# Kernel optimization log

Hardware: AMD Instinct MI355X
Metric: run time of the kernel (lower is better)

The kernel has to match this reference:

```python
import jax, jax.numpy as jnp
import numpy as np

D_MODEL = 1024
N_HEADS = 16
HEAD_DIM = D_MODEL // N_HEADS
ROPE_BASE = 10000.0


def setup_inputs() -> dict:
    key = jax.random.key(0)
    ks = jax.random.split(key, 5)
    B, S = 1, 4096
    scale = 1.0 / np.sqrt(D_MODEL)
    x = jax.random.normal(ks[0], (B, S, D_MODEL), dtype=jnp.float32)
    Wq = jax.random.normal(ks[1], (D_MODEL, D_MODEL), dtype=jnp.float32) * scale
    Wk = jax.random.normal(ks[2], (D_MODEL, D_MODEL), dtype=jnp.float32) * scale
    Wv = jax.random.normal(ks[3], (D_MODEL, D_MODEL), dtype=jnp.float32) * scale
    Wo = jax.random.normal(ks[4], (D_MODEL, D_MODEL), dtype=jnp.float32) * scale
    return {"x": x, "Wq": Wq, "Wk": Wk, "Wv": Wv, "Wo": Wo}


def _rope(q, k):
    # q, k: [B, S, H, Dh]
    S, Dh = q.shape[1], q.shape[-1]
    inv_freq = 1.0 / (ROPE_BASE ** (jnp.arange(0, Dh, 2, dtype=jnp.float32) / Dh))
    t = jnp.arange(S, dtype=jnp.float32)
    freqs = jnp.outer(t, inv_freq)                      # [S, Dh/2]
    emb = jnp.concatenate([freqs, freqs], axis=-1)      # [S, Dh]
    cos = jnp.cos(emb)[None, :, None, :]                # [1, S, 1, Dh]
    sin = jnp.sin(emb)[None, :, None, :]

    def rotate_half(v):
        v1, v2 = v[..., : Dh // 2], v[..., Dh // 2 :]
        return jnp.concatenate([-v2, v1], axis=-1)

    return q * cos + rotate_half(q) * sin, k * cos + rotate_half(k) * sin


def reference(x, Wq, Wk, Wv, Wo):
    B, S, _ = x.shape
    H, Dh = N_HEADS, HEAD_DIM
    # torch Linear: y = x @ W.T
    q = (x @ Wq.T).reshape(B, S, H, Dh)
    k = (x @ Wk.T).reshape(B, S, H, Dh)
    v = (x @ Wv.T).reshape(B, S, H, Dh)
    q, k = _rope(q, k)
    scale = 1.0 / np.sqrt(Dh)
    # scores: [B, H, S, S]
    scores = jnp.einsum("bqhd,bkhd->bhqk", q, k) * scale
    causal = jnp.triu(jnp.ones((S, S), dtype=bool), k=1)
    scores = jnp.where(causal, -jnp.inf, scores)
    attn = jax.nn.softmax(scores, axis=-1)
    out = jnp.einsum("bhqk,bkhd->bqhd", attn, v).reshape(B, S, H * Dh)
    return out @ Wo.T
```

## Files before the change

### kernel.cpp

```cpp
#include <hip/hip_runtime.h>
#include <hip/hip_bf16.h>

typedef __attribute__((ext_vector_type(8))) short bf16x8;
typedef __attribute__((ext_vector_type(4))) float f32x4;
typedef unsigned short u16;

#define S_LEN 4096
#define DM 1024
#define NH 16
#define DH 64
#define PSTR 72

__device__ __forceinline__ u16 f2b_rne(float f) {
  unsigned u = __builtin_bit_cast(unsigned, f);
  return (u16)((u + 0x7fffu + ((u >> 16) & 1u)) >> 16);
}
__device__ __forceinline__ unsigned pk2(float a, float b) {
  unsigned ua = __builtin_bit_cast(unsigned, a);
  unsigned ub = __builtin_bit_cast(unsigned, b);
  ua = (ua + 0x7fffu + ((ua >> 16) & 1u)) >> 16;
  ub = (ub + 0x7fffu + ((ub >> 16) & 1u)) & 0xffff0000u;
  return ua | ub;
}
__device__ __forceinline__ unsigned pk2t(float a, float b) {
  return __builtin_amdgcn_perm(__builtin_bit_cast(unsigned, b),
                               __builtin_bit_cast(unsigned, a), 0x07060302u);
}

__device__ __forceinline__ void glds16(const u16* g, u16* l) {
  __builtin_amdgcn_global_load_lds(
      (const __attribute__((address_space(1))) unsigned int*)g,
      (__attribute__((address_space(3))) unsigned int*)l, 16, 0, 0);
}

__global__ __launch_bounds__(256) void cvt_all(const float* __restrict__ x,
                                               const float* __restrict__ Wq,
                                               const float* __restrict__ Wk,
                                               const float* __restrict__ Wv,
                                               const float* __restrict__ Wo,
                                               u16* __restrict__ xb, u16* __restrict__ wqb,
                                               u16* __restrict__ wkb, u16* __restrict__ wvb,
                                               u16* __restrict__ wob) {
  int idx = (blockIdx.x * 256 + threadIdx.x) * 4;
  const float* src;
  u16* dst;
  int o;
  if (idx < 4194304) {
    src = x; dst = xb; o = idx;
  } else {
    int t = idx - 4194304;
    int wsel = t >> 20;
    o = t & 1048575;
    src = (wsel == 0) ? Wq : (wsel == 1) ? Wk : (wsel == 2) ? Wv : Wo;
    dst = (wsel == 0) ? wqb : (wsel == 1) ? wkb : (wsel == 2) ? wvb : wob;
  }
  float4 v = *(const float4*)(src + o);
  uint2 ov;
  ov.x = pk2(v.x, v.y);
  ov.y = pk2(v.z, v.w);
  *(uint2*)(dst + o) = ov;
}

__global__ __launch_bounds__(256) void zero_kernel(float4* __restrict__ p) {
  p[blockIdx.x * 256 + threadIdx.x] = float4{0.f, 0.f, 0.f, 0.f};
}

__global__ __launch_bounds__(256) void qkv_gemm(const u16* __restrict__ A,
                                                const u16* __restrict__ Wq,
                                                const u16* __restrict__ Wk,
                                                const u16* __restrict__ Wv,
                                                u16* __restrict__ Qo, u16* __restrict__ Ko,
                                                u16* __restrict__ Vt) {
  __shared__ __align__(16) u16 As[2 * 128 * 32];
  __shared__ __align__(16) u16 Bs[2 * 128 * 32];
  const int mat = blockIdx.x >> 3;
  const u16* B = (mat == 0) ? Wq : (mat == 1) ? Wk : Wv;
  const int K = DM, N = DM;
  const int tid = threadIdx.x;
  const int wave = tid >> 6, lane = tid & 63;
  const int fm = lane & 15, fq = lane >> 4;
  const int mb = blockIdx.y * 128, nb = (blockIdx.x & 7) * 128;
  const int wm = (wave & 1) * 64, wn = (wave >> 1) * 64;

  f32x4 acc[4][4];
#pragma unroll
  for (int i = 0; i < 4; ++i)
#pragma unroll
    for (int j = 0; j < 4; ++j)
#pragma unroll
      for (int r = 0; r < 4; ++r) acc[i][j][r] = 0.f;

  const int r_ = tid >> 2;
  const int cg = (tid & 3) ^ ((r_ >> 1) & 3);
  const u16* Ag0 = A + (size_t)(mb + r_) * K + cg * 8;
  const u16* Ag1 = A + (size_t)(mb + r_ + 64) * K + cg * 8;
  const u16* Bg0 = B + (size_t)(nb + r_) * K + cg * 8;
  const u16* Bg1 = B + (size_t)(nb + r_ + 64) * K + cg * 8;
  const int l0 = wave * 512;
  const int l1 = 2048 + wave * 512;
  const int sw = (fm >> 1) & 3;

  int buf = 0;
  glds16(Ag0, As + l0);
  glds16(Ag1, As + l1);
  glds16(Bg0, Bs + l0);
  glds16(Bg1, Bs + l1);

  for (int k0 = 0; k0 < K; k0 += 32) {
    __syncthreads();
    if (k0 + 32 < K) {
      int bo = (buf ^ 1) * 4096;
      glds16(Ag0 + k0 + 32, As + bo + l0);
      glds16(Ag1 + k0 + 32, As + bo + l1);
      glds16(Bg0 + k0 + 32, Bs + bo + l0);
      glds16(Bg1 + k0 + 32, Bs + bo + l1);
    }
    const u16* Ab = As + buf * 4096;
    const u16* Bb = Bs + buf * 4096;
    bf16x8 av[4], bv[4];
#pragma unroll
    for (int t = 0; t < 4; ++t) {
      av[t] = *(const bf16x8*)(Ab + (wm + t * 16 + fm) * 32 + ((fq ^ sw) * 8));
      bv[t] = *(const bf16x8*)(Bb + (wn + t * 16 + fm) * 32 + ((fq ^ sw) * 8));
    }
#pragma unroll
    for (int i = 0; i < 4; ++i)
#pragma unroll
      for (int j = 0; j < 4; ++j)
        acc[i][j] = __builtin_amdgcn_mfma_f32_16x16x32_bf16(av[i], bv[j], acc[i][j], 0, 0, 0);
    buf ^= 1;
  }

  if (mat < 2) {
    u16* Out = (mat == 0) ? Qo : Ko;
    const float qs = (mat == 0) ? 0.1803368801111204f : 1.0f;
    const float c1 = -9.2103403719761836f / 32.f;
    const float if0 = __expf((float)fm * c1);
    const float if1 = __expf((float)(16 + fm) * c1);
#pragma unroll
    for (int ii = 0; ii < 4; ++ii) {
#pragma unroll
      for (int r = 0; r < 4; ++r) {
        float s = (float)(mb + wm + ii * 16 + fq * 4 + r);
#pragma unroll
        for (int jp = 0; jp < 2; ++jp) {
          float ang = s * (jp ? if1 : if0);
          float sn, cs;
          __sincosf(ang, &sn, &cs);
          float a = acc[ii][jp][r], b = acc[ii][jp + 2][r];
          acc[ii][jp][r] = (a * cs - b * sn) * qs;
          acc[ii][jp + 2][r] = (b * cs + a * sn) * qs;
        }
      }
    }
#pragma unroll
    for (int i = 0; i < 4; ++i)
#pragma unroll
      for (int j = 0; j < 4; ++j)
#pragma unroll
        for (int r = 0; r < 4; ++r) {
          int row = mb + wm + i * 16 + fq * 4 + r;
          int col = nb + wn + j * 16 + fm;
          Out[(size_t)row * N + col] = f2b_rne(acc[i][j][r]);
        }
  } else {
#pragma unroll
    for (int i = 0; i < 4; ++i)
#pragma unroll
      for (int j = 0; j < 4; ++j) {
        int col = nb + wn + j * 16 + fm;
        int row0 = mb + wm + i * 16 + fq * 4;
        uint2 pv;
        pv.x = pk2(acc[i][j][0], acc[i][j][1]);
        pv.y = pk2(acc[i][j][2], acc[i][j][3]);
        *(uint2*)(Vt + (size_t)col * S_LEN + row0) = pv;
      }
  }
}

__global__ __launch_bounds__(256) void o_gemm(const u16* __restrict__ A,
                                              const u16* __restrict__ B,
                                              float* __restrict__ C, int M, int N, int K) {
  __shared__ __align__(16) u16 As[2 * 64 * 32];
  __shared__ __align__(16) u16 Bs[2 * 128 * 32];
  const int tid = threadIdx.x;
  const int wave = tid >> 6, lane = tid & 63;
  const int fm = lane & 15, fq = lane >> 4;
  const int mb = blockIdx.y * 64, nb = blockIdx.x * 128;
  const int wm = (wave & 1) * 32, wn = (wave >> 1) * 64;

  f32x4 acc[2][4];
#pragma unroll
  for (int i = 0; i < 2; ++i)
#pragma unroll
    for (int j = 0; j < 4; ++j)
#pragma unroll
      for (int r = 0; r < 4; ++r) acc[i][j][r] = 0.f;

  const int r_ = tid >> 2;
  const int cg = (tid & 3) ^ ((r_ >> 1) & 3);
  const u16* Ag0 = A + (size_t)(mb + r_) * K + cg * 8;
  const u16* Bg0 = B + (size_t)(nb + r_) * K + cg * 8;
  const u16* Bg1 = B + (size_t)(nb + r_ + 64) * K + cg * 8;
  const int l0 = wave * 512;
  const int l1 = 2048 + wave * 512;
  const int sw = (fm >> 1) & 3;

  int buf = 0;
  glds16(Ag0, As + l0);
  glds16(Bg0, Bs + l0);
  glds16(Bg1, Bs + l1);

  for (int k0 = 0; k0 < K; k0 += 32) {
    __syncthreads();
    if (k0 + 32 < K) {
      int aoff = (buf ^ 1) * 2048, boff = (buf ^ 1) * 4096;
      glds16(Ag0 + k0 + 32, As + aoff + l0);
      glds16(Bg0 + k0 + 32, Bs + boff + l0);
      glds16(Bg1 + k0 + 32, Bs + boff + l1);
    }
    const u16* Ab = As + buf * 2048;
    const u16* Bb = Bs + buf * 4096;
    bf16x8 av[2], bv[4];
#pragma unroll
    for (int t = 0; t < 2; ++t)
      av[t] = *(const bf16x8*)(Ab + (wm + t * 16 + fm) * 32 + ((fq ^ sw) * 8));
#pragma unroll
    for (int t = 0; t < 4; ++t)
      bv[t] = *(const bf16x8*)(Bb + (wn + t * 16 + fm) * 32 + ((fq ^ sw) * 8));
#pragma unroll
    for (int i = 0; i < 2; ++i)
#pragma unroll
      for (int j = 0; j < 4; ++j)
        acc[i][j] = __builtin_amdgcn_mfma_f32_16x16x32_bf16(av[i], bv[j], acc[i][j], 0, 0, 0);
    buf ^= 1;
  }
#pragma unroll
  for (int i = 0; i < 2; ++i)
#pragma unroll
    for (int j = 0; j < 4; ++j)
#pragma unroll
      for (int r = 0; r < 4; ++r) {
        int row = mb + wm + i * 16 + fq * 4 + r;
        int col = nb + wn + j * 16 + fm;
        C[(size_t)row * N + col] = acc[i][j][r];
      }
}

template <int STORE>
__global__ __launch_bounds__(512, 4) void attn_kernel(const u16* __restrict__ Q,
                                                      const u16* __restrict__ K,
                                                      const u16* __restrict__ Vt,
                                                      float* __restrict__ Oacc,
                                                      float* __restrict__ Lacc) {
  __shared__ __align__(16) u16 Ks[2 * 4096];
  __shared__ __align__(16) u16 Vs[2 * 4096];
  __shared__ __align__(16) u16 Ps[8][16 * PSTR];
  const int tid = threadIdx.x;
  const int w = tid >> 6, lane = tid & 63;
  const int fm = lane & 15, fq = lane >> 4;
  const int bid = blockIdx.x;
  const int u = bid & 255, hi = bid >> 8;
  const int h = u & 15;
  const int qt0 = u >> 4;
  const int qt = hi ? qt0 : 15 - qt0;
  const int half = hi;
  const int qb = qt * 256 + w * 32;
  const int nlocal = 2 * qt + 2;
  const int kbase = half * nlocal;
  const int dtile = qb >> 6;

  bf16x8 q0[2], q1[2];
#pragma unroll
  for (int g = 0; g < 2; ++g) {
    const u16* qp = Q + (size_t)(qb + g * 16 + fm) * DM + h * DH + fq * 8;
    q0[g] = *(const bf16x8*)(qp);
    q1[g] = *(const bf16x8*)(qp + 32);
  }
  f32x4 o[2][4];
  f32x4 ls[2];
#pragma unroll
  for (int g = 0; g < 2; ++g) {
#pragma unroll
    for (int r = 0; r < 4; ++r) ls[g][r] = 0.f;
#pragma unroll
    for (int c4 = 0; c4 < 4; ++c4)
#pragma unroll
      for (int r = 0; r < 4; ++r) o[g][c4][r] = 0.f;
  }
  const short ONEB = (short)0x3F80;
  const bf16x8 vone = {ONEB, ONEB, ONEB, ONEB, ONEB, ONEB, ONEB, ONEB};

  const int rr = tid >> 3;
  const int cc8 = (tid & 7) ^ (rr & 7);
  const u16* Kg = K + (size_t)rr * DM + h * DH + cc8 * 8;
  const u16* Vg = Vt + (size_t)(h * DH + rr) * S_LEN + cc8 * 8;
  const int l0 = w * 512;
  const int sw7 = fm & 7;
  const f32x4 zf = {0.f, 0.f, 0.f, 0.f};

  glds16(Kg + (size_t)kbase * 64 * DM, Ks + l0);
  glds16(Vg + kbase * 64, Vs + l0);

  int buf = 0;
  for (int kl = 0; kl < nlocal; ++kl) {
    const int ktg = kbase + kl;
    __syncthreads();
    if (kl + 1 < nlocal) {
      int bo = (buf ^ 1) * 4096;
      glds16(Kg + (size_t)(ktg + 1) * 64 * DM, Ks + bo + l0);
      glds16(Vg + (ktg + 1) * 64, Vs + bo + l0);
    }
    if (ktg <= dtile) {
      const u16* Kb = Ks + buf * 4096;
      const u16* Vb = Vs + buf * 4096;

      f32x4 st[2][4];
#pragma unroll
      for (int t = 0; t < 4; ++t) {
        const u16* kr = Kb + (t * 16 + fm) * 64;
        bf16x8 ka = *(const bf16x8*)(kr + ((fq ^ sw7) * 8));
        bf16x8 kb2 = *(const bf16x8*)(kr + (((fq + 4) ^ sw7) * 8));
#pragma unroll
        for (int g = 0; g < 2; ++g) {
          f32x4 s = __builtin_amdgcn_mfma_f32_16x16x32_bf16(ka, q0[g], zf, 0, 0, 0);
          st[g][t] = __builtin_amdgcn_mfma_f32_16x16x32_bf16(kb2, q1[g], s, 0, 0, 0);
        }
      }
      if (ktg == dtile) {
#pragma unroll
        for (int g = 0; g < 2; ++g) {
          int qg = qb + g * 16 + fm;
#pragma unroll
          for (int t = 0; t < 4; ++t) {
            int key = ktg * 64 + t * 16 + fq * 4;
#pragma unroll
            for (int r = 0; r < 4; ++r)
              st[g][t][r] = (key + r > qg) ? -1e30f : st[g][t][r];
          }
        }
      }
      bf16x8 pvb[4][2];
#pragma unroll
      for (int c4 = 0; c4 < 4; ++c4) {
        const u16* vr = Vb + (c4 * 16 + fm) * 64;
        pvb[c4][0] = *(const bf16x8*)(vr + ((fq ^ sw7) * 8));
        pvb[c4][1] = *(const bf16x8*)(vr + (((fq + 4) ^ sw7) * 8));
      }
#pragma unroll
      for (int g = 0; g < 2; ++g) {
#pragma unroll
        for (int t = 0; t < 4; ++t) {
          float p0 = __builtin_amdgcn_exp2f(st[g][t][0]);
          float p1 = __builtin_amdgcn_exp2f(st[g][t][1]);
          float p2 = __builtin_amdgcn_exp2f(st[g][t][2]);
          float p3 = __builtin_amdgcn_exp2f(st[g][t][3]);
          uint2 pk;
          pk.x = pk2t(p0, p1);
          pk.y = pk2t(p2, p3);
          *(uint2*)(&Ps[w][fm * PSTR + t * 16 + fq * 4]) = pk;
        }
        asm volatile("s_waitcnt lgkmcnt(0)" ::: "memory");
        bf16x8 ap0 = *(const bf16x8*)(&Ps[w][fm * PSTR + fq * 8]);
        bf16x8 ap1 = *(const bf16x8*)(&Ps[w][fm * PSTR + 32 + fq * 8]);
        ls[g] = __builtin_amdgcn_mfma_f32_16x16x32_bf16(ap0, vone, ls[g], 0, 0, 0);
        ls[g] = __builtin_amdgcn_mfma_f32_16x16x32_bf16(ap1, vone, ls[g], 0, 0, 0);
#pragma unroll
        for (int c4 = 0; c4 < 4; ++c4) {
          o[g][c4] = __builtin_amdgcn_mfma_f32_16x16x32_bf16(ap0, pvb[c4][0], o[g][c4], 0, 0, 0);
          o[g][c4] = __builtin_amdgcn_mfma_f32_16x16x32_bf16(ap1, pvb[c4][1], o[g][c4], 0, 0, 0);
        }
      }
    }
    buf ^= 1;
  }
  if (STORE) {
    float* Ob = Oacc + (((size_t)half * NH + h) * S_LEN + qt * 256 + w * 32) * DH;
    float* Lb = Lacc + ((size_t)half * NH + h) * S_LEN + qt * 256 + w * 32;
#pragma unroll
    for (int g = 0; g < 2; ++g) {
      if (fm == 0) {
#pragma unroll
        for (int r = 0; r < 4; ++r) Lb[g * 16 + fq * 4 + r] = ls[g][r];
      }
#pragma unroll
      for (int c4 = 0; c4 < 4; ++c4)
#pragma unroll
        for (int r = 0; r < 4; ++r)
          Ob[(size_t)(g * 16 + fq * 4 + r) * DH + c4 * 16 + fm] = o[g][c4][r];
    }
  } else {
    float* Ob = Oacc + ((size_t)h * S_LEN + qt * 256 + w * 32) * DH;
    float* Lb = Lacc + h * S_LEN + qt * 256 + w * 32;
#pragma unroll
    for (int g = 0; g < 2; ++g) {
      if (fm == 0) {
#pragma unroll
        for (int r = 0; r < 4; ++r)
          unsafeAtomicAdd(Lb + g * 16 + fq * 4 + r, ls[g][r]);
      }
#pragma unroll
      for (int c4 = 0; c4 < 4; ++c4)
#pragma unroll
        for (int r = 0; r < 4; ++r)
          unsafeAtomicAdd(Ob + (g * 16 + fq * 4 + r) * DH + c4 * 16 + fm, o[g][c4][r]);
    }
  }
}

__global__ __launch_bounds__(256) void combine2_kernel(const float* __restrict__ O0,
                                                       const float* __restrict__ O1,
                                                       const float* __restrict__ L0,
                                                       const float* __restrict__ L1,
                                                       u16* __restrict__ Ctx) {
  int idx = blockIdx.x * 256 + threadIdx.x;
  int d4 = (idx & 15) * 4;
  int hh = (idx >> 4) & 15;
  int row = idx >> 8;
  size_t ob = ((size_t)hh * S_LEN + row) * DH + d4;
  float4 a = *(const float4*)(O0 + ob);
  float4 b = *(const float4*)(O1 + ob);
  float il = 1.0f / (L0[hh * S_LEN + row] + L1[hh * S_LEN + row]);
  uint2 o;
  o.x = pk2((a.x + b.x) * il, (a.y + b.y) * il);
  o.y = pk2((a.z + b.z) * il, (a.w + b.w) * il);
  *(uint2*)(Ctx + (size_t)row * DM + hh * DH + d4) = o;
}

__global__ __launch_bounds__(256) void combine_kernel(const float* __restrict__ Oacc,
                                                      const float* __restrict__ Lacc,
                                                      u16* __restrict__ Ctx) {
  int idx = blockIdx.x * 256 + threadIdx.x;
  int d4 = (idx & 15) * 4;
  int hh = (idx >> 4) & 15;
  int row = idx >> 8;
  float4 a = *(const float4*)(Oacc + ((size_t)hh * S_LEN + row) * DH + d4);
  float il = 1.0f / Lacc[hh * S_LEN + row];
  uint2 o;
  o.x = pk2(a.x * il, a.y * il);
  o.y = pk2(a.z * il, a.w * il);
  *(uint2*)(Ctx + (size_t)row * DM + hh * DH + d4) = o;
}

extern "C" void kernel_launch(void* const* d_in, const int* in_sizes, int n_in,
                              void* d_out, int out_size, void* d_ws, size_t ws_size,
                              hipStream_t stream) {
  const float* x  = (const float*)d_in[0];
  const float* Wq = (const float*)d_in[1];
  const float* Wk = (const float*)d_in[2];
  const float* Wv = (const float*)d_in[3];
  const float* Wo = (const float*)d_in[4];
  float* out = (float*)d_out;

  const size_t MB = 1u << 20;
  char* ws = (char*)d_ws;

  if (ws_size >= 72 * MB) {
    u16* xb    = (u16*)(ws + 0 * MB);
    u16* wqb   = (u16*)(ws + 8 * MB);
    u16* wkb   = (u16*)(ws + 10 * MB);
    u16* wvb   = (u16*)(ws + 12 * MB);
    u16* wob   = (u16*)(ws + 14 * MB);
    u16* Qb    = (u16*)(ws + 16 * MB);
    u16* Kb    = (u16*)(ws + 24 * MB);
    u16* Vtb   = (u16*)(ws + 32 * MB);
    float* Op  = (float*)(ws + 40 * MB);
    float* Lp  = (float*)(ws + 8 * MB);
    u16* Ctx   = (u16*)(ws + 0 * MB);

    cvt_all<<<8192, 256, 0, stream>>>(x, Wq, Wk, Wv, Wo, xb, wqb, wkb, wvb, wob);
    qkv_gemm<<<dim3(24, 32), 256, 0, stream>>>(xb, wqb, wkb, wvb, Qb, Kb, Vtb);
    attn_kernel<1><<<512, 512, 0, stream>>>(Qb, Kb, Vtb, Op, Lp);
    combine2_kernel<<<4096, 256, 0, stream>>>(Op, Op + (size_t)NH * S_LEN * DH,
                                              Lp, Lp + (size_t)NH * S_LEN, Ctx);
    o_gemm<<<dim3(8, 64), 256, 0, stream>>>(Ctx, wob, out, S_LEN, DM, DM);
  } else {
    u16* xb    = (u16*)(ws + 0 * MB);
    u16* wqb   = (u16*)(ws + 8 * MB);
    u16* wkb   = (u16*)(ws + 10 * MB);
    u16* wvb   = (u16*)(ws + 12 * MB);
    float* Oacc = (float*)(ws + 0 * MB);
    float* Lacc = (float*)(ws + 16 * MB);
    u16* wob   = (u16*)(ws + 17 * MB);
    u16* Qb    = (u16*)(ws + 19 * MB);
    u16* Kb    = (u16*)(ws + 27 * MB);
    u16* Vtb   = (u16*)(ws + 35 * MB);
    u16* Ctx   = (u16*)(ws + 43 * MB);

    cvt_all<<<8192, 256, 0, stream>>>(x, Wq, Wk, Wv, Wo, xb, wqb, wkb, wvb, wob);
    qkv_gemm<<<dim3(24, 32), 256, 0, stream>>>(xb, wqb, wkb, wvb, Qb, Kb, Vtb);
    zero_kernel<<<4160, 256, 0, stream>>>((float4*)Oacc);
    attn_kernel<0><<<512, 512, 0, stream>>>(Qb, Kb, Vtb, Oacc, Lacc);
    combine_kernel<<<4096, 256, 0, stream>>>(Oacc, Lacc, Ctx);
    o_gemm<<<dim3(8, 64), 256, 0, stream>>>(Ctx, wob, out, S_LEN, DM, DM);
  }
}
```

Before: 219.9 us.

## Load K/V fragments directly from global memory instead of LDS double buffer

The attention kernel drops the shared-memory double-buffered K/V staging and its per-iteration block barrier, and instead has each wave load its MFMA operand fragments straight from global memory. Each wave also iterates only up to its own last causal tile, so waves no longer wait on the block for tiles they skip. The trade-off is that the K/V loads, once shared by all eight waves through LDS, are now repeated per wave and served by cache. The loads also have no software prefetch, so global latency is exposed, and the launch-bounds occupancy hint is removed.

```diff
diff --git a/kernel.cpp b/kernel.cpp
--- a/kernel.cpp
+++ b/kernel.cpp
@@ -248,13 +248,11 @@
 }
 
 template <int STORE>
-__global__ __launch_bounds__(512, 4) void attn_kernel(const u16* __restrict__ Q,
-                                                      const u16* __restrict__ K,
-                                                      const u16* __restrict__ Vt,
-                                                      float* __restrict__ Oacc,
-                                                      float* __restrict__ Lacc) {
-  __shared__ __align__(16) u16 Ks[2 * 4096];
-  __shared__ __align__(16) u16 Vs[2 * 4096];
+__global__ __launch_bounds__(512) void attn_kernel(const u16* __restrict__ Q,
+                                                   const u16* __restrict__ K,
+                                                   const u16* __restrict__ Vt,
+                                                   float* __restrict__ Oacc,
+                                                   float* __restrict__ Lacc) {
   __shared__ __align__(16) u16 Ps[8][16 * PSTR];
   const int tid = threadIdx.x;
   const int w = tid >> 6, lane = tid & 63;
@@ -269,6 +267,8 @@
   const int nlocal = 2 * qt + 2;
   const int kbase = half * nlocal;
   const int dtile = qb >> 6;
+  const int kend = kbase + nlocal;
+  const int mylast = (kend - 1 < dtile) ? (kend - 1) : dtile;
 
   bf16x8 q0[2], q1[2];
 #pragma unroll
@@ -290,89 +290,68 @@
   }
   const short ONEB = (short)0x3F80;
   const bf16x8 vone = {ONEB, ONEB, ONEB, ONEB, ONEB, ONEB, ONEB, ONEB};
-
-  const int rr = tid >> 3;
-  const int cc8 = (tid & 7) ^ (rr & 7);
-  const u16* Kg = K + (size_t)rr * DM + h * DH + cc8 * 8;
-  const u16* Vg = Vt + (size_t)(h * DH + rr) * S_LEN + cc8 * 8;
-  const int l0 = w * 512;
-  const int sw7 = fm & 7;
   const f32x4 zf = {0.f, 0.f, 0.f, 0.f};
 
-  glds16(Kg + (size_t)kbase * 64 * DM, Ks + l0);
-  glds16(Vg + kbase * 64, Vs + l0);
-
-  int buf = 0;
-  for (int kl = 0; kl < nlocal; ++kl) {
-    const int ktg = kbase + kl;
-    __syncthreads();
-    if (kl + 1 < nlocal) {
-      int bo = (buf ^ 1) * 4096;
-      glds16(Kg + (size_t)(ktg + 1) * 64 * DM, Ks + bo + l0);
-      glds16(Vg + (ktg + 1) * 64, Vs + bo + l0);
-    }
-    if (ktg <= dtile) {
-      const u16* Kb = Ks + buf * 4096;
-      const u16* Vb = Vs + buf * 4096;
-
-      f32x4 st[2][4];
+  const u16* Kfrag = K + (size_t)fm * DM + h * DH + fq * 8;
+  const u16* Vfrag = Vt + (size_t)(h * DH + fm) * S_LEN + fq * 8;
+
+  for (int ktg = kbase; ktg <= mylast; ++ktg) {
+    f32x4 st[2][4];
+#pragma unroll
+    for (int t = 0; t < 4; ++t) {
+      const u16* kr = Kfrag + (size_t)(ktg * 64 + t * 16) * DM;
+      bf16x8 ka = *(const bf16x8*)(kr);
+      bf16x8 kb2 = *(const bf16x8*)(kr + 32);
+#pragma unroll
+      for (int g = 0; g < 2; ++g) {
+        f32x4 s = __builtin_amdgcn_mfma_f32_16x16x32_bf16(ka, q0[g], zf, 0, 0, 0);
+        st[g][t] = __builtin_amdgcn_mfma_f32_16x16x32_bf16(kb2, q1[g], s, 0, 0, 0);
+      }
+    }
+    if (ktg == dtile) {
+#pragma unroll
+      for (int g = 0; g < 2; ++g) {
+        int qg = qb + g * 16 + fm;
+#pragma unroll
+        for (int t = 0; t < 4; ++t) {
+          int key = ktg * 64 + t * 16 + fq * 4;
+#pragma unroll
+          for (int r = 0; r < 4; ++r)
+            st[g][t][r] = (key + r > qg) ? -1e30f : st[g][t][r];
+        }
+      }
+    }
+    bf16x8 pvb[4][2];
+#pragma unroll
+    for (int c4 = 0; c4 < 4; ++c4) {
+      const u16* vr = Vfrag + (size_t)(c4 * 16) * S_LEN + ktg * 64;
+      pvb[c4][0] = *(const bf16x8*)(vr);
+      pvb[c4][1] = *(const bf16x8*)(vr + 32);
+    }
+#pragma unroll
+    for (int g = 0; g < 2; ++g) {
 #pragma unroll
       for (int t = 0; t < 4; ++t) {
-        const u16* kr = Kb + (t * 16 + fm) * 64;
-        bf16x8 ka = *(const bf16x8*)(kr + ((fq ^ sw7) * 8));
-        bf16x8 kb2 = *(const bf16x8*)(kr + (((fq + 4) ^ sw7) * 8));
-#pragma unroll
-        for (int g = 0; g < 2; ++g) {
-          f32x4 s = __builtin_amdgcn_mfma_f32_16x16x32_bf16(ka, q0[g], zf, 0, 0, 0);
-          st[g][t] = __builtin_amdgcn_mfma_f32_16x16x32_bf16(kb2, q1[g], s, 0, 0, 0);
-        }
-      }
-      if (ktg == dtile) {
-#pragma unroll
-        for (int g = 0; g < 2; ++g) {
-          int qg = qb + g * 16 + fm;
-#pragma unroll
-          for (int t = 0; t < 4; ++t) {
-            int key = ktg * 64 + t * 16 + fq * 4;
-#pragma unroll
-            for (int r = 0; r < 4; ++r)
-              st[g][t][r] = (key + r > qg) ? -1e30f : st[g][t][r];
-          }
-        }
-      }
-      bf16x8 pvb[4][2];
+        float p0 = __builtin_amdgcn_exp2f(st[g][t][0]);
+        float p1 = __builtin_amdgcn_exp2f(st[g][t][1]);
+        float p2 = __builtin_amdgcn_exp2f(st[g][t][2]);
+        float p3 = __builtin_amdgcn_exp2f(st[g][t][3]);
+        uint2 pk;
+        pk.x = pk2t(p0, p1);
+        pk.y = pk2t(p2, p3);
+        *(uint2*)(&Ps[w][fm * PSTR + t * 16 + fq * 4]) = pk;
+      }
+      asm volatile("s_waitcnt lgkmcnt(0)" ::: "memory");
+      bf16x8 ap0 = *(const bf16x8*)(&Ps[w][fm * PSTR + fq * 8]);
+      bf16x8 ap1 = *(const bf16x8*)(&Ps[w][fm * PSTR + 32 + fq * 8]);
+      ls[g] = __builtin_amdgcn_mfma_f32_16x16x32_bf16(ap0, vone, ls[g], 0, 0, 0);
+      ls[g] = __builtin_amdgcn_mfma_f32_16x16x32_bf16(ap1, vone, ls[g], 0, 0, 0);
 #pragma unroll
       for (int c4 = 0; c4 < 4; ++c4) {
-        const u16* vr = Vb + (c4 * 16 + fm) * 64;
-        pvb[c4][0] = *(const bf16x8*)(vr + ((fq ^ sw7) * 8));
-        pvb[c4][1] = *(const bf16x8*)(vr + (((fq + 4) ^ sw7) * 8));
-      }
-#pragma unroll
-      for (int g = 0; g < 2; ++g) {
-#pragma unroll
-        for (int t = 0; t < 4; ++t) {
-          float p0 = __builtin_amdgcn_exp2f(st[g][t][0]);
-          float p1 = __builtin_amdgcn_exp2f(st[g][t][1]);
-          float p2 = __builtin_amdgcn_exp2f(st[g][t][2]);
-          float p3 = __builtin_amdgcn_exp2f(st[g][t][3]);
-          uint2 pk;
-          pk.x = pk2t(p0, p1);
-          pk.y = pk2t(p2, p3);
-          *(uint2*)(&Ps[w][fm * PSTR + t * 16 + fq * 4]) = pk;
-        }
-        asm volatile("s_waitcnt lgkmcnt(0)" ::: "memory");
-        bf16x8 ap0 = *(const bf16x8*)(&Ps[w][fm * PSTR + fq * 8]);
-        bf16x8 ap1 = *(const bf16x8*)(&Ps[w][fm * PSTR + 32 + fq * 8]);
-        ls[g] = __builtin_amdgcn_mfma_f32_16x16x32_bf16(ap0, vone, ls[g], 0, 0, 0);
-        ls[g] = __builtin_amdgcn_mfma_f32_16x16x32_bf16(ap1, vone, ls[g], 0, 0, 0);
-#pragma unroll
-        for (int c4 = 0; c4 < 4; ++c4) {
-          o[g][c4] = __builtin_amdgcn_mfma_f32_16x16x32_bf16(ap0, pvb[c4][0], o[g][c4], 0, 0, 0);
-          o[g][c4] = __builtin_amdgcn_mfma_f32_16x16x32_bf16(ap1, pvb[c4][1], o[g][c4], 0, 0, 0);
-        }
-      }
-    }
-    buf ^= 1;
+        o[g][c4] = __builtin_amdgcn_mfma_f32_16x16x32_bf16(ap0, pvb[c4][0], o[g][c4], 0, 0, 0);
+        o[g][c4] = __builtin_amdgcn_mfma_f32_16x16x32_bf16(ap1, pvb[c4][1], o[g][c4], 0, 0, 0);
+      }
+    }
   }
   if (STORE) {
     float* Ob = Oacc + (((size_t)half * NH + h) * S_LEN + qt * 256 + w * 32) * DH;
```

After: 328.3 us. 49.3% more time.

## Keep softmax probabilities in registers via permuted K row loading

Applied to the files above, without the earlier changes.

K rows are loaded into shared memory in a permuted order, so each lane's QK^T score fragment already matches the operand layout the PV MFMA needs. The probabilities then go straight from registers into the MFMA with operands swapped, instead of a round trip through a per-wave LDS scratch buffer and a wait on LDS. This cuts LDS traffic and shared memory use, which may let more blocks fit per CU. The output now comes out transposed, so stores become float4 row writes; the causal mask key indices are remapped to match the permutation.

```diff
diff --git a/kernel.cpp b/kernel.cpp
--- a/kernel.cpp
+++ b/kernel.cpp
@@ -9,7 +9,6 @@
 #define DM 1024
 #define NH 16
 #define DH 64
-#define PSTR 72
 
 __device__ __forceinline__ u16 f2b_rne(float f) {
   unsigned u = __builtin_bit_cast(unsigned, f);
@@ -255,7 +254,6 @@
                                                       float* __restrict__ Lacc) {
   __shared__ __align__(16) u16 Ks[2 * 4096];
   __shared__ __align__(16) u16 Vs[2 * 4096];
-  __shared__ __align__(16) u16 Ps[8][16 * PSTR];
   const int tid = threadIdx.x;
   const int w = tid >> 6, lane = tid & 63;
   const int fm = lane & 15, fq = lane >> 4;
@@ -293,7 +291,8 @@
 
   const int rr = tid >> 3;
   const int cc8 = (tid & 7) ^ (rr & 7);
-  const u16* Kg = K + (size_t)rr * DM + h * DH + cc8 * 8;
+  const int grr = ((rr >> 5) << 5) | (((rr >> 2) & 3) << 3) | (((rr >> 4) & 1) << 2) | (rr & 3);
+  const u16* Kg = K + (size_t)grr * DM + h * DH + cc8 * 8;
   const u16* Vg = Vt + (size_t)(h * DH + rr) * S_LEN + cc8 * 8;
   const int l0 = w * 512;
   const int sw7 = fm & 7;
@@ -333,7 +332,7 @@
           int qg = qb + g * 16 + fm;
 #pragma unroll
           for (int t = 0; t < 4; ++t) {
-            int key = ktg * 64 + t * 16 + fq * 4;
+            int key = ktg * 64 + (t >> 1) * 32 + fq * 8 + (t & 1) * 4;
 #pragma unroll
             for (int r = 0; r < 4; ++r)
               st[g][t][r] = (key + r > qg) ? -1e30f : st[g][t][r];
@@ -349,26 +348,26 @@
       }
 #pragma unroll
       for (int g = 0; g < 2; ++g) {
+        unsigned pw[8];
 #pragma unroll
         for (int t = 0; t < 4; ++t) {
           float p0 = __builtin_amdgcn_exp2f(st[g][t][0]);
           float p1 = __builtin_amdgcn_exp2f(st[g][t][1]);
           float p2 = __builtin_amdgcn_exp2f(st[g][t][2]);
           float p3 = __builtin_amdgcn_exp2f(st[g][t][3]);
-          uint2 pk;
-          pk.x = pk2t(p0, p1);
-          pk.y = pk2t(p2, p3);
-          *(uint2*)(&Ps[w][fm * PSTR + t * 16 + fq * 4]) = pk;
-        }
-        asm volatile("s_waitcnt lgkmcnt(0)" ::: "memory");
-        bf16x8 ap0 = *(const bf16x8*)(&Ps[w][fm * PSTR + fq * 8]);
-        bf16x8 ap1 = *(const bf16x8*)(&Ps[w][fm * PSTR + 32 + fq * 8]);
-        ls[g] = __builtin_amdgcn_mfma_f32_16x16x32_bf16(ap0, vone, ls[g], 0, 0, 0);
-        ls[g] = __builtin_amdgcn_mfma_f32_16x16x32_bf16(ap1, vone, ls[g], 0, 0, 0);
+          pw[t * 2] = pk2t(p0, p1);
+          pw[t * 2 + 1] = pk2t(p2, p3);
+        }
+        uint4 u0 = {pw[0], pw[1], pw[2], pw[3]};
+        uint4 u1 = {pw[4], pw[5], pw[6], pw[7]};
+        bf16x8 pb0 = __builtin_bit_cast(bf16x8, u0);
+        bf16x8 pb1 = __builtin_bit_cast(bf16x8, u1);
+        ls[g] = __builtin_amdgcn_mfma_f32_16x16x32_bf16(vone, pb0, ls[g], 0, 0, 0);
+        ls[g] = __builtin_amdgcn_mfma_f32_16x16x32_bf16(vone, pb1, ls[g], 0, 0, 0);
 #pragma unroll
         for (int c4 = 0; c4 < 4; ++c4) {
-          o[g][c4] = __builtin_amdgcn_mfma_f32_16x16x32_bf16(ap0, pvb[c4][0], o[g][c4], 0, 0, 0);
-          o[g][c4] = __builtin_amdgcn_mfma_f32_16x16x32_bf16(ap1, pvb[c4][1], o[g][c4], 0, 0, 0);
+          o[g][c4] = __builtin_amdgcn_mfma_f32_16x16x32_bf16(pvb[c4][0], pb0, o[g][c4], 0, 0, 0);
+          o[g][c4] = __builtin_amdgcn_mfma_f32_16x16x32_bf16(pvb[c4][1], pb1, o[g][c4], 0, 0, 0);
         }
       }
     }
@@ -379,31 +378,23 @@
     float* Lb = Lacc + ((size_t)half * NH + h) * S_LEN + qt * 256 + w * 32;
 #pragma unroll
     for (int g = 0; g < 2; ++g) {
-      if (fm == 0) {
-#pragma unroll
-        for (int r = 0; r < 4; ++r) Lb[g * 16 + fq * 4 + r] = ls[g][r];
-      }
+      if (fq == 0) Lb[g * 16 + fm] = ls[g][0];
 #pragma unroll
       for (int c4 = 0; c4 < 4; ++c4)
-#pragma unroll
-        for (int r = 0; r < 4; ++r)
-          Ob[(size_t)(g * 16 + fq * 4 + r) * DH + c4 * 16 + fm] = o[g][c4][r];
+        *(float4*)(Ob + (size_t)(g * 16 + fm) * DH + c4 * 16 + fq * 4) =
+            float4{o[g][c4][0], o[g][c4][1], o[g][c4][2], o[g][c4][3]};
     }
   } else {
     float* Ob = Oacc + ((size_t)h * S_LEN + qt * 256 + w * 32) * DH;
     float* Lb = Lacc + h * S_LEN + qt * 256 + w * 32;
 #pragma unroll
     for (int g = 0; g < 2; ++g) {
-      if (fm == 0) {
+      if (fq == 0) unsafeAtomicAdd(Lb + g * 16 + fm, ls[g][0]);
+#pragma unroll
+      for (int c4 = 0; c4 < 4; ++c4)
 #pragma unroll
         for (int r = 0; r < 4; ++r)
-          unsafeAtomicAdd(Lb + g * 16 + fq * 4 + r, ls[g][r]);
-      }
-#pragma unroll
-      for (int c4 = 0; c4 < 4; ++c4)
-#pragma unroll
-        for (int r = 0; r < 4; ++r)
-          unsafeAtomicAdd(Ob + (g * 16 + fq * 4 + r) * DH + c4 * 16 + fm, o[g][c4][r]);
+          unsafeAtomicAdd(Ob + (size_t)(g * 16 + fm) * DH + c4 * 16 + fq * 4 + r, o[g][c4][r]);
     }
   }
 }
```

Measured after the change: 199.3 us. 1.1x faster.
